# Performance work log

Measured on AMD Instinct MI355X. Metric: run time of the kernel, lower is better.

The kernel has to match this reference:

```python
import jax, jax.numpy as jnp
import numpy as np

NEG_NUM = -10000.0

def setup_inputs() -> dict:
    key = jax.random.key(0)
    k1, k2, k3, k4, k5, k6 = jax.random.split(key, 6)
    batch, enc_len = 32, 2048
    ctx_size, query_size, att_hid = 1024, 1024, 512
    in_dim = ctx_size + query_size
    ctx = jax.random.normal(k1, (batch, enc_len, ctx_size), dtype=jnp.float32)
    query = jax.random.normal(k2, (batch, query_size), dtype=jnp.float32)
    mask = jax.random.randint(k3, (batch, enc_len), 0, 2, dtype=jnp.int32)
    # Linear params (stored as (in, out) for x @ W + b)
    s1 = 1.0 / np.sqrt(in_dim)
    W1 = jax.random.uniform(k4, (in_dim, att_hid), jnp.float32, -s1, s1)
    b1 = jnp.zeros((att_hid,), jnp.float32)
    s2 = 1.0 / np.sqrt(att_hid)
    W2 = jax.random.uniform(k5, (att_hid, 1), jnp.float32, -s2, s2)
    b2 = jnp.zeros((1,), jnp.float32)
    return {"ctx": ctx, "query": query, "W1": W1, "b1": b1, "W2": W2, "b2": b2, "mask": mask}

def reference(ctx, query, W1, b1, W2, b2, mask):
    # ctx: (B, S, Dc), query: (B, Dq)
    B, S, Dc = ctx.shape
    Dq = query.shape[-1]
    # Equivalent to concat([ctx, query_expanded]) @ W1: split W1 into ctx/query blocks
    Wc, Wq = W1[:Dc], W1[Dc:]
    hidden = jnp.tanh(jnp.einsum('bsd,dh->bsh', ctx, Wc)
                      + (query @ Wq)[:, None, :] + b1)      # (B, S, H)
    score = jnp.einsum('bsh,h->bs', hidden, W2[:, 0]) + b2[0]  # (B, S)
    score = jnp.where(mask == 0, NEG_NUM, score)
    p_ctx = jax.nn.softmax(score, axis=-1)                   # (B, S)
    expected_ctx = jnp.einsum('bs,bsd->bd', p_ctx, ctx)      # (B, Dc)
    return (expected_ctx, p_ctx)
```

## Files before the change

### kernel.cpp

```cpp
#include <hip/hip_runtime.h>

typedef __bf16 bf16;
typedef __attribute__((ext_vector_type(8))) __bf16 bf16x8;
typedef __attribute__((ext_vector_type(4))) __bf16 bf16x4;
typedef __attribute__((ext_vector_type(4))) float f32x4;

#define B_  32
#define S_  2048
#define DC  1024
#define DQ  1024
#define H_  512
#define M_  (B_*S_)

#define BM  128
#define BN  512
#define BK  32
#define NCH 32

#define GLD16(g, l) __builtin_amdgcn_global_load_lds( \
    (__attribute__((address_space(1))) void*)(g),     \
    (__attribute__((address_space(3))) void*)(l), 16, 0, 0)

__global__ __launch_bounds__(256) void k_prep(const float* __restrict__ W1,
                                              const float* __restrict__ query,
                                              const float* __restrict__ b1,
                                              bf16* __restrict__ WcT2,
                                              float* __restrict__ qb) {
    const int bid = blockIdx.x, tid = threadIdx.x;
    if (bid < 256) {
        __shared__ bf16 t[32 * 68];
        const int kb = bid >> 3;
        const int cb = bid & 7;
        #pragma unroll
        for (int i = 0; i < 2; ++i) {
            int idx = i * 256 + tid;
            int k  = idx >> 4;
            int h4 = (idx & 15) * 4;
            const float4 v = *(const float4*)(W1 + ((size_t)(kb * 32 + k)) * H_ + cb * 64 + h4);
            bf16x4 pk = { (bf16)v.x, (bf16)v.y, (bf16)v.z, (bf16)v.w };
            *(bf16x4*)(&t[k * 68 + h4]) = pk;
        }
        __syncthreads();
        const int col = tid >> 2;
        const int kk0 = (tid & 3) * 8;
        bf16x8 o;
        #pragma unroll
        for (int j = 0; j < 8; ++j) o[j] = t[(kk0 + j) * 68 + col];
        *(bf16x8*)(WcT2 + (size_t)kb * 16384 + (size_t)(cb * 64 + col) * 32 + kk0) = o;
    } else {
        const int r = bid - 256;
        const int hblk = r & 7;
        const int b    = r >> 3;
        __shared__ float q[DQ];
        __shared__ float red[256];
        #pragma unroll
        for (int i = 0; i < 4; ++i)
            q[tid + i * 256] = query[(size_t)b * DQ + tid + i * 256];
        __syncthreads();
        const int h  = hblk * 64 + (tid & 63);
        const int kc = tid >> 6;
        const float* w = W1 + (size_t)DC * H_ + (size_t)(kc * 256) * H_ + h;
        const float* qv = q + kc * 256;
        float acc = 0.0f;
        #pragma unroll 8
        for (int k = 0; k < 256; ++k)
            acc = fmaf(qv[k], w[(size_t)k * H_], acc);
        red[tid] = acc;
        __syncthreads();
        if (tid < 64)
            qb[(size_t)b * H_ + hblk * 64 + tid] =
                red[tid] + red[tid + 64] + red[tid + 128] + red[tid + 192] + b1[hblk * 64 + tid];
    }
}

__global__ __launch_bounds__(512) void k_gemm(const float* __restrict__ ctx,
                                              const bf16*  __restrict__ WcT2,
                                              const float* __restrict__ qb,
                                              const float* __restrict__ W2,
                                              float* __restrict__ score) {
    __shared__ char smem_raw[81920];
    bf16* As = (bf16*)smem_raw;
    bf16* Bs = (bf16*)(smem_raw + 16384);
    float* red = (float*)smem_raw;

    const int tid  = threadIdx.x;
    const int mblk = blockIdx.x;
    const size_t row_base = (size_t)mblk * BM;
    const int b = mblk >> 4;

    const int lane = tid & 63;
    const int wave = tid >> 6;
    const int wm   = wave & 1;
    const int wn   = wave >> 1;
    const int l16  = lane & 15;
    const int quad = lane >> 4;

    f32x4 acc[4][8] = {};

    const int am = tid >> 2;
    const int ak = (tid & 3) << 3;
    const float* actx = ctx + (row_base + am) * (size_t)DC + ak;
    const int aoff = am * BK + ak;
    const bf16* bsrc = WcT2 + tid * 8;
    const int boff = tid * 8;
    const int fA = (wm * 64 + l16) * BK + quad * 8;
    const int fB = (wn * 128 + l16) * BK + quad * 8;

    {
        const float4 v0 = *(const float4*)(actx);
        const float4 v1 = *(const float4*)(actx + 4);
        bf16x8 a8 = { (bf16)v0.x, (bf16)v0.y, (bf16)v0.z, (bf16)v0.w,
                      (bf16)v1.x, (bf16)v1.y, (bf16)v1.z, (bf16)v1.w };
        *(bf16x8*)(As + aoff) = a8;
        #pragma unroll
        for (int i = 0; i < 4; ++i)
            GLD16(bsrc + i * 4096, Bs + boff + i * 4096);
    }
    __syncthreads();

    for (int kb = 0; kb < DC / BK; ++kb) {
        const int cur = kb & 1, nxt = cur ^ 1;
        float4 av0, av1;
        if (kb < 31) {
            #pragma unroll
            for (int i = 0; i < 4; ++i)
                GLD16(bsrc + (size_t)(kb + 1) * 16384 + i * 4096,
                      Bs + nxt * 16384 + boff + i * 4096);
            av0 = *(const float4*)(actx + (kb + 1) * BK);
            av1 = *(const float4*)(actx + (kb + 1) * BK + 4);
        }

        bf16x8 aF[4], bF[8];
        const bf16* aP = As + cur * 4096 + fA;
        const bf16* bP = Bs + cur * 16384 + fB;
        #pragma unroll
        for (int mf = 0; mf < 4; ++mf) aF[mf] = *(const bf16x8*)(aP + mf * (16 * BK));
        #pragma unroll
        for (int nf = 0; nf < 8; ++nf) bF[nf] = *(const bf16x8*)(bP + nf * (16 * BK));
        #pragma unroll
        for (int mf = 0; mf < 4; ++mf)
            #pragma unroll
            for (int nf = 0; nf < 8; ++nf)
                acc[mf][nf] = __builtin_amdgcn_mfma_f32_16x16x32_bf16(aF[mf], bF[nf], acc[mf][nf], 0, 0, 0);

        if (kb < 31) {
            bf16x8 a8 = { (bf16)av0.x, (bf16)av0.y, (bf16)av0.z, (bf16)av0.w,
                          (bf16)av1.x, (bf16)av1.y, (bf16)av1.z, (bf16)av1.w };
            *(bf16x8*)(As + nxt * 4096 + aoff) = a8;
        }
        __syncthreads();
    }

    float qv[8], wv[8];
    #pragma unroll
    for (int nf = 0; nf < 8; ++nf) {
        int c = wn * 128 + nf * 16 + l16;
        qv[nf] = qb[(size_t)b * H_ + c];
        wv[nf] = W2[c];
    }
    #pragma unroll
    for (int mf = 0; mf < 4; ++mf) {
        #pragma unroll
        for (int r = 0; r < 4; ++r) {
            float s = 0.0f;
            #pragma unroll
            for (int nf = 0; nf < 8; ++nf) {
                float x = acc[mf][nf][r] + qv[nf];
                float t = 1.0f - 2.0f / (1.0f + __expf(2.0f * x));
                s = fmaf(t, wv[nf], s);
            }
            s += __shfl_xor(s, 1);
            s += __shfl_xor(s, 2);
            s += __shfl_xor(s, 4);
            s += __shfl_xor(s, 8);
            if (l16 == 0)
                red[(wm * 64 + mf * 16 + quad * 4 + r) * 4 + wn] = s;
        }
    }
    __syncthreads();
    if (tid < BM)
        score[row_base + tid] = red[tid * 4] + red[tid * 4 + 1] + red[tid * 4 + 2] + red[tid * 4 + 3];
}

__global__ __launch_bounds__(256) void k_softmax(const float* __restrict__ score,
                                                 const float* __restrict__ b2,
                                                 const int*   __restrict__ mask,
                                                 float* __restrict__ p_out) {
    int b = blockIdx.x, tid = threadIdx.x;
    __shared__ float red[256];
    float loc[8];
    float b2v = b2[0];
    float mx = -1e30f;
    #pragma unroll
    for (int i = 0; i < 8; ++i) {
        size_t r = (size_t)b * S_ + i * 256 + tid;
        float v = score[r] + b2v;
        if (mask[r] == 0) v = -10000.0f;
        loc[i] = v;
        mx = fmaxf(mx, v);
    }
    red[tid] = mx; __syncthreads();
    for (int o = 128; o > 0; o >>= 1) {
        if (tid < o) red[tid] = fmaxf(red[tid], red[tid + o]);
        __syncthreads();
    }
    mx = red[0]; __syncthreads();
    float se = 0.0f;
    #pragma unroll
    for (int i = 0; i < 8; ++i) {
        float e = __expf(loc[i] - mx);
        loc[i] = e;
        se += e;
    }
    red[tid] = se; __syncthreads();
    for (int o = 128; o > 0; o >>= 1) {
        if (tid < o) red[tid] += red[tid + o];
        __syncthreads();
    }
    float inv = 1.0f / red[0];
    #pragma unroll
    for (int i = 0; i < 8; ++i)
        p_out[(size_t)b * S_ + i * 256 + tid] = loc[i] * inv;
}

__global__ __launch_bounds__(256) void k_expected(const float* __restrict__ ctx,
                                                  const float* __restrict__ p,
                                                  float* __restrict__ partial) {
    int b = blockIdx.x, ch = blockIdx.y, tid = threadIdx.x;
    __shared__ float ps[64];
    if (tid < 64) ps[tid] = p[(size_t)b * S_ + ch * 64 + tid];
    __syncthreads();
    const float* base = ctx + ((size_t)b * S_ + ch * 64) * DC + tid * 4;
    float ax = 0.f, ay = 0.f, az = 0.f, aw = 0.f;
    #pragma unroll 8
    for (int s = 0; s < 64; ++s) {
        const float4 v = *(const float4*)(base + (size_t)s * DC);
        float w = ps[s];
        ax = fmaf(w, v.x, ax);
        ay = fmaf(w, v.y, ay);
        az = fmaf(w, v.z, az);
        aw = fmaf(w, v.w, aw);
    }
    float4 o = { ax, ay, az, aw };
    *(float4*)(partial + ((size_t)(b * NCH + ch)) * DC + tid * 4) = o;
}

__global__ __launch_bounds__(256) void k_reduce(const float* __restrict__ partial,
                                                float* __restrict__ out) {
    int b = blockIdx.x, tid = threadIdx.x;
    float4 acc = { 0.f, 0.f, 0.f, 0.f };
    #pragma unroll
    for (int c = 0; c < NCH; ++c) {
        const float4 v = *(const float4*)(partial + ((size_t)(b * NCH + c)) * DC + tid * 4);
        acc.x += v.x; acc.y += v.y; acc.z += v.z; acc.w += v.w;
    }
    *(float4*)(out + (size_t)b * DC + tid * 4) = acc;
}

extern "C" void kernel_launch(void* const* d_in, const int* in_sizes, int n_in,
                              void* d_out, int out_size, void* d_ws, size_t ws_size,
                              hipStream_t stream) {
    (void)in_sizes; (void)n_in; (void)out_size; (void)ws_size;
    const float* ctx   = (const float*)d_in[0];
    const float* query = (const float*)d_in[1];
    const float* W1    = (const float*)d_in[2];
    const float* b1    = (const float*)d_in[3];
    const float* W2    = (const float*)d_in[4];
    const float* b2    = (const float*)d_in[5];
    const int*   mask  = (const int*)d_in[6];

    float* out      = (float*)d_out;
    float* expected = out;
    float* p_out    = out + 32768;

    char* w = (char*)d_ws;
    bf16*  WcT2      = (bf16*)w;
    float* qb        = (float*)(w + (1 << 20));
    float* score     = (float*)(w + (1 << 20) + (64 << 10));
    float* partial_e = (float*)(w + (1 << 20) + (320 << 10));

    k_prep    <<<512, 256, 0, stream>>>(W1, query, b1, WcT2, qb);
    k_gemm    <<<512, 512, 0, stream>>>(ctx, WcT2, qb, W2, score);
    k_softmax <<<B_, 256, 0, stream>>>(score, b2, mask, p_out);
    k_expected<<<dim3(B_, NCH), 256, 0, stream>>>(ctx, p_out, partial_e);
    k_reduce  <<<B_, 256, 0, stream>>>(partial_e, expected);
}
```

Measured before the change: 493.9 us.

## Fuse softmax with expected-context, cache bf16 ctx copy from GEMM

The GEMM now uses 64-row tiles with 256 threads and, when workspace allows, writes a bf16 copy of ctx while converting it. A new fused kernel computes softmax and the weighted context sum per (batch, 128-column) block, reading the bf16 copy, which replaces the separate softmax, partial, and reduce kernels. This halves the bytes read in the second ctx pass but adds a 128 MB bf16 write, recomputes softmax 8 times per batch, launches only 256 blocks for the reduction, and lowers the precision of expected_ctx.

```diff
diff --git a/kernel.cpp b/kernel.cpp
--- a/kernel.cpp
+++ b/kernel.cpp
@@ -12,10 +12,9 @@
 #define H_  512
 #define M_  (B_*S_)
 
-#define BM  128
+#define BM  64
 #define BN  512
 #define BK  32
-#define NCH 32
 
 #define GLD16(g, l) __builtin_amdgcn_global_load_lds( \
     (__attribute__((address_space(1))) void*)(g),     \
@@ -73,25 +72,25 @@
     }
 }
 
-__global__ __launch_bounds__(512) void k_gemm(const float* __restrict__ ctx,
+template<bool STORE>
+__global__ __launch_bounds__(256) void k_gemm(const float* __restrict__ ctx,
                                               const bf16*  __restrict__ WcT2,
                                               const float* __restrict__ qb,
                                               const float* __restrict__ W2,
-                                              float* __restrict__ score) {
-    __shared__ char smem_raw[81920];
-    bf16* As = (bf16*)smem_raw;
-    bf16* Bs = (bf16*)(smem_raw + 16384);
-    float* red = (float*)smem_raw;
+                                              float* __restrict__ score,
+                                              bf16* __restrict__ ctxb) {
+    __shared__ char smem[73728];
+    bf16* As = (bf16*)smem;
+    bf16* Bs = (bf16*)(smem + 8192);
+    float* red = (float*)smem;
 
     const int tid  = threadIdx.x;
     const int mblk = blockIdx.x;
     const size_t row_base = (size_t)mblk * BM;
-    const int b = mblk >> 4;
+    const int b = mblk >> 5;
 
     const int lane = tid & 63;
-    const int wave = tid >> 6;
-    const int wm   = wave & 1;
-    const int wn   = wave >> 1;
+    const int wn   = tid >> 6;
     const int l16  = lane & 15;
     const int quad = lane >> 4;
 
@@ -100,10 +99,11 @@
     const int am = tid >> 2;
     const int ak = (tid & 3) << 3;
     const float* actx = ctx + (row_base + am) * (size_t)DC + ak;
-    const int aoff = am * BK + ak;
+    bf16* actxb = STORE ? (ctxb + (row_base + am) * (size_t)DC + ak) : (bf16*)nullptr;
+    const int aoff = tid * 8;
     const bf16* bsrc = WcT2 + tid * 8;
     const int boff = tid * 8;
-    const int fA = (wm * 64 + l16) * BK + quad * 8;
+    const int fA = l16 * BK + quad * 8;
     const int fB = (wn * 128 + l16) * BK + quad * 8;
 
     {
@@ -112,9 +112,10 @@
         bf16x8 a8 = { (bf16)v0.x, (bf16)v0.y, (bf16)v0.z, (bf16)v0.w,
                       (bf16)v1.x, (bf16)v1.y, (bf16)v1.z, (bf16)v1.w };
         *(bf16x8*)(As + aoff) = a8;
-        #pragma unroll
-        for (int i = 0; i < 4; ++i)
-            GLD16(bsrc + i * 4096, Bs + boff + i * 4096);
+        if (STORE) *(bf16x8*)actxb = a8;
+        #pragma unroll
+        for (int i = 0; i < 8; ++i)
+            GLD16(bsrc + i * 2048, Bs + boff + i * 2048);
     }
     __syncthreads();
 
@@ -123,15 +124,15 @@
         float4 av0, av1;
         if (kb < 31) {
             #pragma unroll
-            for (int i = 0; i < 4; ++i)
-                GLD16(bsrc + (size_t)(kb + 1) * 16384 + i * 4096,
-                      Bs + nxt * 16384 + boff + i * 4096);
+            for (int i = 0; i < 8; ++i)
+                GLD16(bsrc + (size_t)(kb + 1) * 16384 + i * 2048,
+                      Bs + nxt * 16384 + boff + i * 2048);
             av0 = *(const float4*)(actx + (kb + 1) * BK);
             av1 = *(const float4*)(actx + (kb + 1) * BK + 4);
         }
 
         bf16x8 aF[4], bF[8];
-        const bf16* aP = As + cur * 4096 + fA;
+        const bf16* aP = As + cur * 2048 + fA;
         const bf16* bP = Bs + cur * 16384 + fB;
         #pragma unroll
         for (int mf = 0; mf < 4; ++mf) aF[mf] = *(const bf16x8*)(aP + mf * (16 * BK));
@@ -146,7 +147,8 @@
         if (kb < 31) {
             bf16x8 a8 = { (bf16)av0.x, (bf16)av0.y, (bf16)av0.z, (bf16)av0.w,
                           (bf16)av1.x, (bf16)av1.y, (bf16)av1.z, (bf16)av1.w };
-            *(bf16x8*)(As + nxt * 4096 + aoff) = a8;
+            *(bf16x8*)(As + nxt * 2048 + aoff) = a8;
+            if (STORE) *(bf16x8*)(actxb + (kb + 1) * BK) = a8;
         }
         __syncthreads();
     }
@@ -174,7 +176,7 @@
             s += __shfl_xor(s, 4);
             s += __shfl_xor(s, 8);
             if (l16 == 0)
-                red[(wm * 64 + mf * 16 + quad * 4 + r) * 4 + wn] = s;
+                red[(mf * 16 + quad * 4 + r) * 4 + wn] = s;
         }
     }
     __syncthreads();
@@ -182,19 +184,26 @@
         score[row_base + tid] = red[tid * 4] + red[tid * 4 + 1] + red[tid * 4 + 2] + red[tid * 4 + 3];
 }
 
-__global__ __launch_bounds__(256) void k_softmax(const float* __restrict__ score,
-                                                 const float* __restrict__ b2,
-                                                 const int*   __restrict__ mask,
-                                                 float* __restrict__ p_out) {
-    int b = blockIdx.x, tid = threadIdx.x;
+template<bool BF>
+__global__ __launch_bounds__(256) void k_exp(const float* __restrict__ score,
+                                             const float* __restrict__ b2p,
+                                             const int*   __restrict__ mask,
+                                             const float* __restrict__ ctxf,
+                                             const bf16*  __restrict__ ctxb,
+                                             float* __restrict__ expected,
+                                             float* __restrict__ p_out) {
+    const int hblk = blockIdx.x, b = blockIdx.y, tid = threadIdx.x;
+    __shared__ float ps[S_];
     __shared__ float red[256];
+    __shared__ float red2[8 * 32 * 4];
+
+    const float b2 = b2p[0];
     float loc[8];
-    float b2v = b2[0];
     float mx = -1e30f;
     #pragma unroll
     for (int i = 0; i < 8; ++i) {
         size_t r = (size_t)b * S_ + i * 256 + tid;
-        float v = score[r] + b2v;
+        float v = score[r] + b2;
         if (mask[r] == 0) v = -10000.0f;
         loc[i] = v;
         mx = fmaxf(mx, v);
@@ -209,7 +218,7 @@
     #pragma unroll
     for (int i = 0; i < 8; ++i) {
         float e = __expf(loc[i] - mx);
-        loc[i] = e;
+        ps[i * 256 + tid] = e;
         se += e;
     }
     red[tid] = se; __syncthreads();
@@ -217,50 +226,60 @@
         if (tid < o) red[tid] += red[tid + o];
         __syncthreads();
     }
-    float inv = 1.0f / red[0];
-    #pragma unroll
-    for (int i = 0; i < 8; ++i)
-        p_out[(size_t)b * S_ + i * 256 + tid] = loc[i] * inv;
-}
-
-__global__ __launch_bounds__(256) void k_expected(const float* __restrict__ ctx,
-                                                  const float* __restrict__ p,
-                                                  float* __restrict__ partial) {
-    int b = blockIdx.x, ch = blockIdx.y, tid = threadIdx.x;
-    __shared__ float ps[64];
-    if (tid < 64) ps[tid] = p[(size_t)b * S_ + ch * 64 + tid];
+    const float inv = 1.0f / red[0];
     __syncthreads();
-    const float* base = ctx + ((size_t)b * S_ + ch * 64) * DC + tid * 4;
-    float ax = 0.f, ay = 0.f, az = 0.f, aw = 0.f;
-    #pragma unroll 8
-    for (int s = 0; s < 64; ++s) {
-        const float4 v = *(const float4*)(base + (size_t)s * DC);
-        float w = ps[s];
-        ax = fmaf(w, v.x, ax);
-        ay = fmaf(w, v.y, ay);
-        az = fmaf(w, v.z, az);
-        aw = fmaf(w, v.w, aw);
-    }
-    float4 o = { ax, ay, az, aw };
-    *(float4*)(partial + ((size_t)(b * NCH + ch)) * DC + tid * 4) = o;
-}
-
-__global__ __launch_bounds__(256) void k_reduce(const float* __restrict__ partial,
-                                                float* __restrict__ out) {
-    int b = blockIdx.x, tid = threadIdx.x;
-    float4 acc = { 0.f, 0.f, 0.f, 0.f };
-    #pragma unroll
-    for (int c = 0; c < NCH; ++c) {
-        const float4 v = *(const float4*)(partial + ((size_t)(b * NCH + c)) * DC + tid * 4);
-        acc.x += v.x; acc.y += v.y; acc.z += v.z; acc.w += v.w;
-    }
-    *(float4*)(out + (size_t)b * DC + tid * 4) = acc;
+    if (hblk == 0) {
+        #pragma unroll
+        for (int i = 0; i < 8; ++i)
+            p_out[(size_t)b * S_ + i * 256 + tid] = ps[i * 256 + tid] * inv;
+    }
+
+    const int c4  = (tid & 31) * 4;
+    const int rg  = tid >> 5;
+    const int col0 = hblk * 128;
+    float a0 = 0.f, a1 = 0.f, a2 = 0.f, a3 = 0.f;
+    if (BF) {
+        const bf16* base = ctxb + ((size_t)b * S_ + rg) * DC + col0 + c4;
+        #pragma unroll 4
+        for (int s0 = 0; s0 < S_; s0 += 8) {
+            float w = ps[s0 + rg];
+            bf16x4 v = *(const bf16x4*)(base + (size_t)s0 * DC);
+            a0 = fmaf(w, (float)v[0], a0);
+            a1 = fmaf(w, (float)v[1], a1);
+            a2 = fmaf(w, (float)v[2], a2);
+            a3 = fmaf(w, (float)v[3], a3);
+        }
+    } else {
+        const float* base = ctxf + ((size_t)b * S_ + rg) * DC + col0 + c4;
+        #pragma unroll 4
+        for (int s0 = 0; s0 < S_; s0 += 8) {
+            float w = ps[s0 + rg];
+            const float4 v = *(const float4*)(base + (size_t)s0 * DC);
+            a0 = fmaf(w, v.x, a0);
+            a1 = fmaf(w, v.y, a1);
+            a2 = fmaf(w, v.z, a2);
+            a3 = fmaf(w, v.w, a3);
+        }
+    }
+    float* r2 = &red2[(rg * 32 + (tid & 31)) * 4];
+    r2[0] = a0; r2[1] = a1; r2[2] = a2; r2[3] = a3;
+    __syncthreads();
+    if (tid < 32) {
+        float s0 = 0.f, s1 = 0.f, s2 = 0.f, s3 = 0.f;
+        #pragma unroll
+        for (int g = 0; g < 8; ++g) {
+            const float* q = &red2[(g * 32 + tid) * 4];
+            s0 += q[0]; s1 += q[1]; s2 += q[2]; s3 += q[3];
+        }
+        float4 o = { s0 * inv, s1 * inv, s2 * inv, s3 * inv };
+        *(float4*)(expected + (size_t)b * DC + col0 + tid * 4) = o;
+    }
 }
 
 extern "C" void kernel_launch(void* const* d_in, const int* in_sizes, int n_in,
                               void* d_out, int out_size, void* d_ws, size_t ws_size,
                               hipStream_t stream) {
-    (void)in_sizes; (void)n_in; (void)out_size; (void)ws_size;
+    (void)in_sizes; (void)n_in; (void)out_size;
     const float* ctx   = (const float*)d_in[0];
     const float* query = (const float*)d_in[1];
     const float* W1    = (const float*)d_in[2];
@@ -273,15 +292,24 @@
     float* expected = out;
     float* p_out    = out + 32768;
 
+    const size_t CTXB_BYTES = (size_t)M_ * DC * sizeof(bf16);
+    const size_t need = CTXB_BYTES + (1 << 20) + (64 << 10) + (256 << 10) + 256;
     char* w = (char*)d_ws;
-    bf16*  WcT2      = (bf16*)w;
-    float* qb        = (float*)(w + (1 << 20));
-    float* score     = (float*)(w + (1 << 20) + (64 << 10));
-    float* partial_e = (float*)(w + (1 << 20) + (320 << 10));
-
-    k_prep    <<<512, 256, 0, stream>>>(W1, query, b1, WcT2, qb);
-    k_gemm    <<<512, 512, 0, stream>>>(ctx, WcT2, qb, W2, score);
-    k_softmax <<<B_, 256, 0, stream>>>(score, b2, mask, p_out);
-    k_expected<<<dim3(B_, NCH), 256, 0, stream>>>(ctx, p_out, partial_e);
-    k_reduce  <<<B_, 256, 0, stream>>>(partial_e, expected);
+
+    if (ws_size >= need) {
+        bf16*  ctxb  = (bf16*)w;
+        bf16*  WcT2  = (bf16*)(w + CTXB_BYTES);
+        float* qb    = (float*)(w + CTXB_BYTES + (1 << 20));
+        float* score = (float*)(w + CTXB_BYTES + (1 << 20) + (64 << 10));
+        k_prep      <<<512, 256, 0, stream>>>(W1, query, b1, WcT2, qb);
+        k_gemm<true><<<M_ / BM, 256, 0, stream>>>(ctx, WcT2, qb, W2, score, ctxb);
+        k_exp<true> <<<dim3(8, B_), 256, 0, stream>>>(score, b2, mask, ctx, ctxb, expected, p_out);
+    } else {
+        bf16*  WcT2  = (bf16*)w;
+        float* qb    = (float*)(w + (1 << 20));
+        float* score = (float*)(w + (1 << 20) + (64 << 10));
+        k_prep       <<<512, 256, 0, stream>>>(W1, query, b1, WcT2, qb);
+        k_gemm<false><<<M_ / BM, 256, 0, stream>>>(ctx, WcT2, qb, W2, score, nullptr);
+        k_exp<false> <<<dim3(8, B_), 256, 0, stream>>>(score, b2, mask, ctx, nullptr, expected, p_out);
+    }
 }
```

Measured after the change: 512.1 us. +3.7%, slower.

## Drop LDS staging in GEMM; load fragments directly from global into registers

Applied to the files above, without the earlier changes.

The score GEMM no longer stages tiles in shared memory. Each wave now loads its A fragments (ctx, converted to bf16) and B fragments (pre-transposed W1) straight from global memory into registers, prefetching A one step ahead. Block size drops from 128 rows and 512 threads to 64 rows and 256 threads, with two blocks per CU, removing per-iteration barriers and LDS traffic. The cost is that B is reloaded by every block and A is reloaded by every wave, so global and L2 load traffic rises a lot. The expected-context and reduce kernels also get a reordered grid and finer-grained parallelism in the reduction.

```diff
diff --git a/kernel.cpp b/kernel.cpp
--- a/kernel.cpp
+++ b/kernel.cpp
@@ -12,14 +12,7 @@
 #define H_  512
 #define M_  (B_*S_)
 
-#define BM  128
-#define BN  512
-#define BK  32
-#define NCH 32
-
-#define GLD16(g, l) __builtin_amdgcn_global_load_lds( \
-    (__attribute__((address_space(1))) void*)(g),     \
-    (__attribute__((address_space(3))) void*)(l), 16, 0, 0)
+#define BM  64
 
 __global__ __launch_bounds__(256) void k_prep(const float* __restrict__ W1,
                                               const float* __restrict__ query,
@@ -73,82 +66,64 @@
     }
 }
 
-__global__ __launch_bounds__(512) void k_gemm(const float* __restrict__ ctx,
-                                              const bf16*  __restrict__ WcT2,
-                                              const float* __restrict__ qb,
-                                              const float* __restrict__ W2,
-                                              float* __restrict__ score) {
-    __shared__ char smem_raw[81920];
-    bf16* As = (bf16*)smem_raw;
-    bf16* Bs = (bf16*)(smem_raw + 16384);
-    float* red = (float*)smem_raw;
+__global__ __launch_bounds__(256, 2) void k_gemm(const float* __restrict__ ctx,
+                                                 const bf16*  __restrict__ WcT2,
+                                                 const float* __restrict__ qb,
+                                                 const float* __restrict__ W2,
+                                                 float* __restrict__ score) {
+    __shared__ float red[BM * 4];
 
     const int tid  = threadIdx.x;
     const int mblk = blockIdx.x;
     const size_t row_base = (size_t)mblk * BM;
-    const int b = mblk >> 4;
+    const int b = mblk >> 5;
 
     const int lane = tid & 63;
-    const int wave = tid >> 6;
-    const int wm   = wave & 1;
-    const int wn   = wave >> 1;
+    const int wn   = tid >> 6;
     const int l16  = lane & 15;
     const int quad = lane >> 4;
 
     f32x4 acc[4][8] = {};
 
-    const int am = tid >> 2;
-    const int ak = (tid & 3) << 3;
-    const float* actx = ctx + (row_base + am) * (size_t)DC + ak;
-    const int aoff = am * BK + ak;
-    const bf16* bsrc = WcT2 + tid * 8;
-    const int boff = tid * 8;
-    const int fA = (wm * 64 + l16) * BK + quad * 8;
-    const int fB = (wn * 128 + l16) * BK + quad * 8;
-
-    {
-        const float4 v0 = *(const float4*)(actx);
-        const float4 v1 = *(const float4*)(actx + 4);
-        bf16x8 a8 = { (bf16)v0.x, (bf16)v0.y, (bf16)v0.z, (bf16)v0.w,
-                      (bf16)v1.x, (bf16)v1.y, (bf16)v1.z, (bf16)v1.w };
-        *(bf16x8*)(As + aoff) = a8;
-        #pragma unroll
-        for (int i = 0; i < 4; ++i)
-            GLD16(bsrc + i * 4096, Bs + boff + i * 4096);
-    }
-    __syncthreads();
-
-    for (int kb = 0; kb < DC / BK; ++kb) {
+    const float* arow[4];
+    #pragma unroll
+    for (int mf = 0; mf < 4; ++mf)
+        arow[mf] = ctx + (row_base + mf * 16 + l16) * (size_t)DC + quad * 8;
+    const bf16* bptr = WcT2 + (size_t)(wn * 128 + l16) * 32 + quad * 8;
+
+    float4 av0[2][4], av1[2][4];
+    #pragma unroll
+    for (int mf = 0; mf < 4; ++mf) {
+        av0[0][mf] = *(const float4*)(arow[mf]);
+        av1[0][mf] = *(const float4*)(arow[mf] + 4);
+    }
+
+    #pragma unroll 2
+    for (int kb = 0; kb < 32; ++kb) {
         const int cur = kb & 1, nxt = cur ^ 1;
-        float4 av0, av1;
+        bf16x8 bF[8];
+        #pragma unroll
+        for (int nf = 0; nf < 8; ++nf)
+            bF[nf] = *(const bf16x8*)(bptr + (size_t)kb * 16384 + nf * 512);
         if (kb < 31) {
             #pragma unroll
-            for (int i = 0; i < 4; ++i)
-                GLD16(bsrc + (size_t)(kb + 1) * 16384 + i * 4096,
-                      Bs + nxt * 16384 + boff + i * 4096);
-            av0 = *(const float4*)(actx + (kb + 1) * BK);
-            av1 = *(const float4*)(actx + (kb + 1) * BK + 4);
-        }
-
-        bf16x8 aF[4], bF[8];
-        const bf16* aP = As + cur * 4096 + fA;
-        const bf16* bP = Bs + cur * 16384 + fB;
-        #pragma unroll
-        for (int mf = 0; mf < 4; ++mf) aF[mf] = *(const bf16x8*)(aP + mf * (16 * BK));
-        #pragma unroll
-        for (int nf = 0; nf < 8; ++nf) bF[nf] = *(const bf16x8*)(bP + nf * (16 * BK));
+            for (int mf = 0; mf < 4; ++mf) {
+                av0[nxt][mf] = *(const float4*)(arow[mf] + (kb + 1) * 32);
+                av1[nxt][mf] = *(const float4*)(arow[mf] + (kb + 1) * 32 + 4);
+            }
+        }
+        bf16x8 aF[4];
+        #pragma unroll
+        for (int mf = 0; mf < 4; ++mf) {
+            const float4 v0 = av0[cur][mf], v1 = av1[cur][mf];
+            aF[mf] = bf16x8{ (bf16)v0.x, (bf16)v0.y, (bf16)v0.z, (bf16)v0.w,
+                             (bf16)v1.x, (bf16)v1.y, (bf16)v1.z, (bf16)v1.w };
+        }
         #pragma unroll
         for (int mf = 0; mf < 4; ++mf)
             #pragma unroll
             for (int nf = 0; nf < 8; ++nf)
                 acc[mf][nf] = __builtin_amdgcn_mfma_f32_16x16x32_bf16(aF[mf], bF[nf], acc[mf][nf], 0, 0, 0);
-
-        if (kb < 31) {
-            bf16x8 a8 = { (bf16)av0.x, (bf16)av0.y, (bf16)av0.z, (bf16)av0.w,
-                          (bf16)av1.x, (bf16)av1.y, (bf16)av1.z, (bf16)av1.w };
-            *(bf16x8*)(As + nxt * 4096 + aoff) = a8;
-        }
-        __syncthreads();
     }
 
     float qv[8], wv[8];
@@ -174,7 +149,7 @@
             s += __shfl_xor(s, 4);
             s += __shfl_xor(s, 8);
             if (l16 == 0)
-                red[(wm * 64 + mf * 16 + quad * 4 + r) * 4 + wn] = s;
+                red[(mf * 16 + quad * 4 + r) * 4 + wn] = s;
         }
     }
     __syncthreads();
@@ -226,11 +201,11 @@
 __global__ __launch_bounds__(256) void k_expected(const float* __restrict__ ctx,
                                                   const float* __restrict__ p,
                                                   float* __restrict__ partial) {
-    int b = blockIdx.x, ch = blockIdx.y, tid = threadIdx.x;
+    const int sb = blockIdx.x, b = blockIdx.y, tid = threadIdx.x;
     __shared__ float ps[64];
-    if (tid < 64) ps[tid] = p[(size_t)b * S_ + ch * 64 + tid];
+    if (tid < 64) ps[tid] = p[(size_t)b * S_ + sb * 64 + tid];
     __syncthreads();
-    const float* base = ctx + ((size_t)b * S_ + ch * 64) * DC + tid * 4;
+    const float* base = ctx + ((size_t)b * S_ + sb * 64) * DC + tid * 4;
     float ax = 0.f, ay = 0.f, az = 0.f, aw = 0.f;
     #pragma unroll 8
     for (int s = 0; s < 64; ++s) {
@@ -242,19 +217,18 @@
         aw = fmaf(w, v.w, aw);
     }
     float4 o = { ax, ay, az, aw };
-    *(float4*)(partial + ((size_t)(b * NCH + ch)) * DC + tid * 4) = o;
+    *(float4*)(partial + ((size_t)(b * 32 + sb)) * DC + tid * 4) = o;
 }
 
 __global__ __launch_bounds__(256) void k_reduce(const float* __restrict__ partial,
                                                 float* __restrict__ out) {
-    int b = blockIdx.x, tid = threadIdx.x;
-    float4 acc = { 0.f, 0.f, 0.f, 0.f };
-    #pragma unroll
-    for (int c = 0; c < NCH; ++c) {
-        const float4 v = *(const float4*)(partial + ((size_t)(b * NCH + c)) * DC + tid * 4);
-        acc.x += v.x; acc.y += v.y; acc.z += v.z; acc.w += v.w;
-    }
-    *(float4*)(out + (size_t)b * DC + tid * 4) = acc;
+    const int cq = blockIdx.x, b = blockIdx.y, tid = threadIdx.x;
+    const int c = cq * 256 + tid;
+    float acc = 0.f;
+    #pragma unroll
+    for (int sb = 0; sb < 32; ++sb)
+        acc += partial[((size_t)(b * 32 + sb)) * DC + c];
+    out[(size_t)b * DC + c] = acc;
 }
 
 extern "C" void kernel_launch(void* const* d_in, const int* in_sizes, int n_in,
@@ -280,8 +254,8 @@
     float* partial_e = (float*)(w + (1 << 20) + (320 << 10));
 
     k_prep    <<<512, 256, 0, stream>>>(W1, query, b1, WcT2, qb);
-    k_gemm    <<<512, 512, 0, stream>>>(ctx, WcT2, qb, W2, score);
+    k_gemm    <<<M_ / BM, 256, 0, stream>>>(ctx, WcT2, qb, W2, score);
     k_softmax <<<B_, 256, 0, stream>>>(score, b2, mask, p_out);
-    k_expected<<<dim3(B_, NCH), 256, 0, stream>>>(ctx, p_out, partial_e);
-    k_reduce  <<<B_, 256, 0, stream>>>(partial_e, expected);
-}
+    k_expected<<<dim3(32, B_), 256, 0, stream>>>(ctx, p_out, partial_e);
+    k_reduce  <<<dim3(4, B_), 256, 0, stream>>>(partial_e, expected);
+}
```

After: 550.6 us. 11.5% more time.
